# Optimization experiments

Hardware: AMD Instinct MI355X
Metric: run time of the kernel (lower is better)

## Reference

```python
import jax, jax.numpy as jnp
import numpy as np

B, T, C, H = 4, 4096, 512, 64  # batch, seq(patches), n_embed, head_size

def setup_inputs() -> dict:
    key = jax.random.key(0)
    kx, kk, kq, kv = jax.random.split(key, 4)
    x = jax.random.normal(kx, (B, T, C), dtype=jnp.float32)
    # torch nn.Linear(n_embed, head_size).weight is [H, C]; store transposed [C, H]
    Wk = jax.random.normal(kk, (C, H), dtype=jnp.float32) / np.sqrt(C)
    Wq = jax.random.normal(kq, (C, H), dtype=jnp.float32) / np.sqrt(C)
    Wv = jax.random.normal(kv, (C, H), dtype=jnp.float32) / np.sqrt(C)
    return {"x": x, "Wk": Wk, "Wq": Wq, "Wv": Wv}

def reference(x, Wk, Wq, Wv):
    Bn, Tn, Cn = x.shape
    k = x @ Wk  # [B,T,H]
    q = x @ Wq
    v = x @ Wv
    # NOTE: original scales by C**-0.5 with C = n_embed (input dim), not head_size
    scores = jnp.einsum('bth,bsh->bts', q, k) * (Cn ** -0.5)  # [B,T,T]
    causal = jnp.tril(jnp.ones((Tn, Tn), dtype=bool))
    scores = jnp.where(causal, scores, -jnp.inf)
    attn = jax.nn.softmax(scores, axis=-1)
    return jnp.einsum('bts,bsh->bth', attn, v)  # [B,T,H]
```

## Files before the change

kernel.cpp:

```cpp
#include <hip/hip_runtime.h>
#include <hip/hip_bf16.h>

#define Bb 4
#define Tt 4096

typedef __bf16 bf16;
typedef __attribute__((ext_vector_type(8))) __bf16 bf16x8;
typedef __attribute__((ext_vector_type(4))) __bf16 bf16x4;
typedef __attribute__((ext_vector_type(2))) __bf16 bf16x2;
typedef __attribute__((ext_vector_type(4))) float f32x4;
typedef __attribute__((ext_vector_type(2))) unsigned int u32x2;
typedef __attribute__((ext_vector_type(4))) unsigned int u32x4;


__global__ __launch_bounds__(256) void wt_kernel(const float* __restrict__ Wk,
                                                 const float* __restrict__ Wq,
                                                 const float* __restrict__ Wv,
                                                 bf16* __restrict__ wt) {
  int idx = blockIdx.x * 256 + threadIdx.x;
  int mat = idx >> 15;
  int rem = idx & 32767;
  int n = rem >> 9;
  int k = rem & 511;
  const float* W = (mat == 0) ? Wk : (mat == 1) ? Wq : Wv;
  float v = W[k * 64 + n];
  if (mat == 1) v *= 0.0637587165f;
  wt[idx] = (bf16)v;
}

__global__ __launch_bounds__(256) void proj_kernel(const float* __restrict__ x,
                                                   const bf16* __restrict__ wt,
                                                   bf16* __restrict__ Kb,
                                                   bf16* __restrict__ Qb,
                                                   bf16* __restrict__ VTb) {
  __shared__ __attribute__((aligned(16))) bf16 xs[16][520];
  int tid = threadIdx.x;
  int row0 = blockIdx.x * 16;

  int sr = tid >> 4, sc = (tid & 15) * 4;
  const float* xr = x + (size_t)(row0 + sr) * 512;
#pragma unroll
  for (int j = 0; j < 8; ++j) {
    f32x4 a = *(const f32x4*)(xr + sc + j * 64);
    bf16x4 h;
#pragma unroll
    for (int e = 0; e < 4; ++e) h[e] = (bf16)a[e];
    *(bf16x4*)&xs[sr][sc + j * 64] = h;
  }
  __syncthreads();

  int wave = tid >> 6, lane = tid & 63, m = lane & 15, quad = lane >> 4;
  f32x4 acc[3];
#pragma unroll
  for (int i = 0; i < 3; ++i) acc[i] = (f32x4){0.f, 0.f, 0.f, 0.f};

#pragma unroll 4
  for (int kk = 0; kk < 512; kk += 32) {
    bf16x8 af = *(const bf16x8*)&xs[m][kk + quad * 8];
#pragma unroll
    for (int i = 0; i < 3; ++i) {
      int nt = wave * 3 + i;
      bf16x8 bfr = *(const bf16x8*)(wt + (nt >> 2) * 32768 +
                                    (((nt & 3) * 16) + m) * 512 + kk + quad * 8);
      acc[i] = __builtin_amdgcn_mfma_f32_16x16x32_bf16(af, bfr, acc[i], 0, 0, 0);
    }
  }

  int b = row0 >> 12, tloc = row0 & 4095;
#pragma unroll
  for (int i = 0; i < 3; ++i) {
    int nt = wave * 3 + i, mat = nt >> 2, n0 = (nt & 3) * 16;
    if (mat == 2) {
      bf16x4 pv;
#pragma unroll
      for (int r = 0; r < 4; ++r) pv[r] = (bf16)acc[i][r];
      *(bf16x4*)&VTb[((size_t)b * 64 + n0 + m) * 4096 + tloc + quad * 4] = pv;
    } else {
      bf16* dst = (mat == 0) ? Kb : Qb;
#pragma unroll
      for (int r = 0; r < 4; ++r)
        dst[(size_t)(row0 + quad * 4 + r) * 64 + n0 + m] = (bf16)acc[i][r];
    }
  }
}

static __device__ inline unsigned pk2(float lo, float hi) {
  bf16x2 t;
  t[0] = (bf16)lo;
  t[1] = (bf16)hi;
  return __builtin_bit_cast(unsigned int, t);
}
static __device__ inline void plswap(unsigned& a, unsigned& b) {
  u32x2 r = __builtin_amdgcn_permlane16_swap(a, b, false, false);
  a = r.x;
  b = r.y;
}

__global__ __launch_bounds__(256, 4) void attn_kernel(const bf16* __restrict__ Qb,
                                                      const bf16* __restrict__ Kb,
                                                      const bf16* __restrict__ VTb,
                                                      bf16* __restrict__ Opart,
                                                      float* __restrict__ Lpart,
                                                      float* __restrict__ out) {
  __shared__ __attribute__((aligned(16))) bf16 Kt[2][64][72];
  __shared__ __attribute__((aligned(16))) bf16 Vt[2][64][72];

  int tid = threadIdx.x, wave = tid >> 6, lane = tid & 63;
  int m = lane & 15, quad = lane >> 4, kq = quad * 8;

  int uu = 1151 - (int)blockIdx.x;
  int b = uu / 288, u2 = uu % 288;
  int g = 0;
  while (u2 >= 4 * (g + 1) * (g + 2)) ++g;
  int rr = u2 - 4 * g * (g + 1);
  int qi = 8 * g + rr / (g + 1);
  int c = rr % (g + 1);
  int t0 = qi * 64;
  int s_beg = c * 512;
  int s_end = min(s_beg + 512, t0 + 64);
  int niter = (s_end - s_beg) >> 6;

  const bf16* Qp = Qb + ((size_t)b * Tt + t0 + wave * 16 + m) * 64;
  bf16x8 aq0 = *(const bf16x8*)(Qp + kq);
  bf16x8 aq1 = *(const bf16x8*)(Qp + 32 + kq);

  bf16x8 onesb;
#pragma unroll
  for (int j = 0; j < 8; ++j) onesb[j] = (bf16)1.0f;

  f32x4 o[4];
#pragma unroll
  for (int i = 0; i < 4; ++i) o[i] = (f32x4){0.f, 0.f, 0.f, 0.f};
  f32x4 lsum = (f32x4){0.f, 0.f, 0.f, 0.f};

  int r_ = tid >> 2, seg = tid & 3;
  const bf16* Kbase = Kb + (size_t)b * Tt * 64;
  const bf16* VTbase = VTb + (size_t)b * 64 * 4096;

  {
    const bf16* ks = Kbase + (size_t)(s_beg + r_) * 64 + seg * 16;
    bf16x8 k0 = *(const bf16x8*)ks;
    bf16x8 k1 = *(const bf16x8*)(ks + 8);
    const bf16* vs = VTbase + (size_t)r_ * 4096 + s_beg + seg * 16;
    bf16x8 v0 = *(const bf16x8*)vs;
    bf16x8 v1 = *(const bf16x8*)(vs + 8);
    *(bf16x8*)&Kt[0][r_][seg * 16] = k0;
    *(bf16x8*)&Kt[0][r_][seg * 16 + 8] = k1;
    *(bf16x8*)&Vt[0][r_][seg * 16] = v0;
    *(bf16x8*)&Vt[0][r_][seg * 16 + 8] = v1;
  }
  __syncthreads();

  int qrow = t0 + wave * 16 + m;

  for (int i = 0; i < niter; ++i) {
    int s0 = s_beg + i * 64;
    int cb = i & 1;
    bool more = (i + 1 < niter);

    bf16x8 k0, k1, v0, v1;
    if (more) {
      int sn = s0 + 64;
      const bf16* ks2 = Kbase + (size_t)(sn + r_) * 64 + seg * 16;
      k0 = *(const bf16x8*)ks2;
      k1 = *(const bf16x8*)(ks2 + 8);
      const bf16* vs2 = VTbase + (size_t)r_ * 4096 + sn + seg * 16;
      v0 = *(const bf16x8*)vs2;
      v1 = *(const bf16x8*)(vs2 + 8);
    }

    f32x4 s[4];
#pragma unroll
    for (int nt = 0; nt < 4; ++nt) {
      bf16x8 ak0 = *(const bf16x8*)&Kt[cb][nt * 16 + m][kq];
      bf16x8 ak1 = *(const bf16x8*)&Kt[cb][nt * 16 + m][32 + kq];
      f32x4 sa = (f32x4){0.f, 0.f, 0.f, 0.f};
      sa = __builtin_amdgcn_mfma_f32_16x16x32_bf16(ak0, aq0, sa, 0, 0, 0);
      sa = __builtin_amdgcn_mfma_f32_16x16x32_bf16(ak1, aq1, sa, 0, 0, 0);
      s[nt] = sa;
    }

    if (s0 + 64 > t0) {
      int kvb = s0 + 4 * quad;
#pragma unroll
      for (int nt = 0; nt < 4; ++nt)
#pragma unroll
        for (int r = 0; r < 4; ++r)
          if (kvb + nt * 16 + r > qrow) s[nt][r] = -1e30f;
    }

    unsigned pA[4], pB[4];
#pragma unroll
    for (int nt = 0; nt < 4; ++nt) {
      float e0 = __builtin_amdgcn_exp2f(s[nt][0]);
      float e1 = __builtin_amdgcn_exp2f(s[nt][1]);
      float e2 = __builtin_amdgcn_exp2f(s[nt][2]);
      float e3 = __builtin_amdgcn_exp2f(s[nt][3]);
      pA[nt] = pk2(e0, e1);
      pB[nt] = pk2(e2, e3);
    }

#pragma unroll
    for (int ch = 0; ch < 2; ++ch) {
      unsigned a0 = pA[2 * ch], a1 = pA[2 * ch + 1];
      unsigned c0 = pB[2 * ch], c1 = pB[2 * ch + 1];
      plswap(a0, a1);
      plswap(c0, c1);
      u32x4 uap = {a0, c0, a1, c1};
      bf16x8 ap = __builtin_bit_cast(bf16x8, uap);
      lsum = __builtin_amdgcn_mfma_f32_16x16x32_bf16(ap, onesb, lsum, 0, 0, 0);
      int fb8 = (4 * ch + 2 * (quad & 1) + (quad >> 1)) * 8;
#pragma unroll
      for (int nt = 0; nt < 4; ++nt) {
        bf16x8 bv = *(const bf16x8*)&Vt[cb][nt * 16 + m][fb8];
        o[nt] = __builtin_amdgcn_mfma_f32_16x16x32_bf16(ap, bv, o[nt], 0, 0, 0);
      }
    }

    if (more) {
      int nb = cb ^ 1;
      *(bf16x8*)&Kt[nb][r_][seg * 16] = k0;
      *(bf16x8*)&Kt[nb][r_][seg * 16 + 8] = k1;
      *(bf16x8*)&Vt[nb][r_][seg * 16] = v0;
      *(bf16x8*)&Vt[nb][r_][seg * 16 + 8] = v1;
      __syncthreads();
    }
  }

  int rl0 = wave * 16 + quad * 4;
  if (qi < 8) {
    float* op = out + ((size_t)b * Tt + t0) * 64;
#pragma unroll
    for (int r = 0; r < 4; ++r) {
      float inv = 1.0f / lsum[r];
#pragma unroll
      for (int nt = 0; nt < 4; ++nt)
        op[(size_t)(rl0 + r) * 64 + nt * 16 + m] = o[nt][r] * inv;
    }
  } else {
    int p = b * 288 + 4 * g * (g + 1) + (qi - 8 * g) * (g + 1) + c;
    bf16* Op = Opart + (size_t)p * 4096;
#pragma unroll
    for (int r = 0; r < 4; ++r)
#pragma unroll
      for (int nt = 0; nt < 4; ++nt)
        Op[(rl0 + r) * 64 + nt * 16 + m] = (bf16)o[nt][r];
    if (m == 0) {
#pragma unroll
      for (int r = 0; r < 4; ++r) Lpart[p * 64 + rl0 + r] = lsum[r];
    }
  }
}

__global__ __launch_bounds__(256) void combine_kernel(const bf16* __restrict__ Opart,
                                                      const float* __restrict__ Lpart,
                                                      float* __restrict__ out) {
  int blk = blockIdx.x;
  int b = blk / 224, rem = blk % 224;
  int qi = 8 + (rem >> 2), rq = rem & 3;
  int g = qi >> 3, nc = g + 1;
  int pb = b * 288 + 4 * g * (g + 1) + (qi - 8 * g) * (g + 1);
  int t = threadIdx.x, col = t & 63, rl = t >> 6;
#pragma unroll
  for (int rr = 0; rr < 4; ++rr) {
    int row64 = rq * 16 + rl * 4 + rr;
    float L = 0.f, acc = 0.f;
    for (int cc = 0; cc < nc; ++cc) {
      L += Lpart[(pb + cc) * 64 + row64];
      acc += (float)Opart[(size_t)(pb + cc) * 4096 + row64 * 64 + col];
    }
    out[((size_t)b * Tt + qi * 64 + row64) * 64 + col] = acc / L;
  }
}

extern "C" void kernel_launch(void* const* d_in, const int* in_sizes, int n_in,
                              void* d_out, int out_size, void* d_ws, size_t ws_size,
                              hipStream_t stream) {
  const float* x = (const float*)d_in[0];
  const float* Wk = (const float*)d_in[1];
  const float* Wq = (const float*)d_in[2];
  const float* Wv = (const float*)d_in[3];
  float* out = (float*)d_out;

  char* w = (char*)d_ws;
  bf16* wt = (bf16*)w;
  bf16* Kb = (bf16*)(w + 196608);
  bf16* Qb = (bf16*)(w + 2293760);
  bf16* VTb = (bf16*)(w + 4390912);
  bf16* Opart = (bf16*)(w + 6488064);
  float* Lpart = (float*)(w + 15925248);

  wt_kernel<<<384, 256, 0, stream>>>(Wk, Wq, Wv, wt);
  proj_kernel<<<1024, 256, 0, stream>>>(x, wt, Kb, Qb, VTb);
  attn_kernel<<<1152, 256, 0, stream>>>(Qb, Kb, VTb, Opart, Lpart, out);
  combine_kernel<<<896, 256, 0, stream>>>(Opart, Lpart, out);
}
```

Before: 134.4 us.

## Process two 64-row query tiles per attention block to reuse K/V tiles

Measured after the change: 131.7 us. 2.0% less time.

```diff
diff --git a/kernel.cpp b/kernel.cpp
--- a/kernel.cpp
+++ b/kernel.cpp
@@ -96,7 +96,7 @@
   b = r.y;
 }
 
-__global__ __launch_bounds__(256, 4) void attn_kernel(const bf16* __restrict__ Qb,
+__global__ __launch_bounds__(256, 3) void attn_kernel(const bf16* __restrict__ Qb,
                                                       const bf16* __restrict__ Kb,
                                                       const bf16* __restrict__ VTb,
                                                       bf16* __restrict__ Opart,
@@ -108,30 +108,36 @@
   int tid = threadIdx.x, wave = tid >> 6, lane = tid & 63;
   int m = lane & 15, quad = lane >> 4, kq = quad * 8;
 
-  int uu = 1151 - (int)blockIdx.x;
-  int b = uu / 288, u2 = uu % 288;
+  int uu = 575 - (int)blockIdx.x;
+  int b = uu / 144, u2 = uu % 144;
   int g = 0;
-  while (u2 >= 4 * (g + 1) * (g + 2)) ++g;
-  int rr = u2 - 4 * g * (g + 1);
-  int qi = 8 * g + rr / (g + 1);
+  while (u2 >= 2 * (g + 1) * (g + 2)) ++g;
+  int rr = u2 - 2 * g * (g + 1);
+  int qi2 = 4 * g + rr / (g + 1);
   int c = rr % (g + 1);
-  int t0 = qi * 64;
+  int t0 = qi2 * 128;
   int s_beg = c * 512;
-  int s_end = min(s_beg + 512, t0 + 64);
+  int s_end = min(s_beg + 512, t0 + 128);
   int niter = (s_end - s_beg) >> 6;
 
   const bf16* Qp = Qb + ((size_t)b * Tt + t0 + wave * 16 + m) * 64;
-  bf16x8 aq0 = *(const bf16x8*)(Qp + kq);
-  bf16x8 aq1 = *(const bf16x8*)(Qp + 32 + kq);
+  bf16x8 aq00 = *(const bf16x8*)(Qp + kq);
+  bf16x8 aq01 = *(const bf16x8*)(Qp + 32 + kq);
+  bf16x8 aq10 = *(const bf16x8*)(Qp + 4096 + kq);
+  bf16x8 aq11 = *(const bf16x8*)(Qp + 4096 + 32 + kq);
 
   bf16x8 onesb;
 #pragma unroll
   for (int j = 0; j < 8; ++j) onesb[j] = (bf16)1.0f;
 
-  f32x4 o[4];
-#pragma unroll
-  for (int i = 0; i < 4; ++i) o[i] = (f32x4){0.f, 0.f, 0.f, 0.f};
-  f32x4 lsum = (f32x4){0.f, 0.f, 0.f, 0.f};
+  f32x4 o0[4], o1[4];
+#pragma unroll
+  for (int i = 0; i < 4; ++i) {
+    o0[i] = (f32x4){0.f, 0.f, 0.f, 0.f};
+    o1[i] = (f32x4){0.f, 0.f, 0.f, 0.f};
+  }
+  f32x4 lsum0 = (f32x4){0.f, 0.f, 0.f, 0.f};
+  f32x4 lsum1 = (f32x4){0.f, 0.f, 0.f, 0.f};
 
   int r_ = tid >> 2, seg = tid & 3;
   const bf16* Kbase = Kb + (size_t)b * Tt * 64;
@@ -151,16 +157,16 @@
   }
   __syncthreads();
 
-  int qrow = t0 + wave * 16 + m;
+  int qrow0 = t0 + wave * 16 + m;
 
   for (int i = 0; i < niter; ++i) {
-    int s0 = s_beg + i * 64;
+    int kv0 = s_beg + i * 64;
     int cb = i & 1;
     bool more = (i + 1 < niter);
 
     bf16x8 k0, k1, v0, v1;
     if (more) {
-      int sn = s0 + 64;
+      int sn = kv0 + 64;
       const bf16* ks2 = Kbase + (size_t)(sn + r_) * 64 + seg * 16;
       k0 = *(const bf16x8*)ks2;
       k1 = *(const bf16x8*)(ks2 + 8);
@@ -169,52 +175,76 @@
       v1 = *(const bf16x8*)(vs2 + 8);
     }
 
-    f32x4 s[4];
+    f32x4 s0[4], s1[4];
 #pragma unroll
     for (int nt = 0; nt < 4; ++nt) {
       bf16x8 ak0 = *(const bf16x8*)&Kt[cb][nt * 16 + m][kq];
       bf16x8 ak1 = *(const bf16x8*)&Kt[cb][nt * 16 + m][32 + kq];
       f32x4 sa = (f32x4){0.f, 0.f, 0.f, 0.f};
-      sa = __builtin_amdgcn_mfma_f32_16x16x32_bf16(ak0, aq0, sa, 0, 0, 0);
-      sa = __builtin_amdgcn_mfma_f32_16x16x32_bf16(ak1, aq1, sa, 0, 0, 0);
-      s[nt] = sa;
-    }
-
-    if (s0 + 64 > t0) {
-      int kvb = s0 + 4 * quad;
+      sa = __builtin_amdgcn_mfma_f32_16x16x32_bf16(ak0, aq00, sa, 0, 0, 0);
+      sa = __builtin_amdgcn_mfma_f32_16x16x32_bf16(ak1, aq01, sa, 0, 0, 0);
+      s0[nt] = sa;
+      f32x4 sb = (f32x4){0.f, 0.f, 0.f, 0.f};
+      sb = __builtin_amdgcn_mfma_f32_16x16x32_bf16(ak0, aq10, sb, 0, 0, 0);
+      sb = __builtin_amdgcn_mfma_f32_16x16x32_bf16(ak1, aq11, sb, 0, 0, 0);
+      s1[nt] = sb;
+    }
+
+    if (kv0 + 64 > t0) {
+      int kvb = kv0 + 4 * quad;
 #pragma unroll
       for (int nt = 0; nt < 4; ++nt)
 #pragma unroll
         for (int r = 0; r < 4; ++r)
-          if (kvb + nt * 16 + r > qrow) s[nt][r] = -1e30f;
-    }
-
-    unsigned pA[4], pB[4];
+          if (kvb + nt * 16 + r > qrow0) s0[nt][r] = -1e30f;
+    }
+    if (kv0 >= t0 + 64) {
+      int kvb = kv0 + 4 * quad;
+#pragma unroll
+      for (int nt = 0; nt < 4; ++nt)
+#pragma unroll
+        for (int r = 0; r < 4; ++r)
+          if (kvb + nt * 16 + r > qrow0 + 64) s1[nt][r] = -1e30f;
+    }
+
+    unsigned pA0[4], pB0[4], pA1[4], pB1[4];
 #pragma unroll
     for (int nt = 0; nt < 4; ++nt) {
-      float e0 = __builtin_amdgcn_exp2f(s[nt][0]);
-      float e1 = __builtin_amdgcn_exp2f(s[nt][1]);
-      float e2 = __builtin_amdgcn_exp2f(s[nt][2]);
-      float e3 = __builtin_amdgcn_exp2f(s[nt][3]);
-      pA[nt] = pk2(e0, e1);
-      pB[nt] = pk2(e2, e3);
+      pA0[nt] = pk2(__builtin_amdgcn_exp2f(s0[nt][0]), __builtin_amdgcn_exp2f(s0[nt][1]));
+      pB0[nt] = pk2(__builtin_amdgcn_exp2f(s0[nt][2]), __builtin_amdgcn_exp2f(s0[nt][3]));
+      pA1[nt] = pk2(__builtin_amdgcn_exp2f(s1[nt][0]), __builtin_amdgcn_exp2f(s1[nt][1]));
+      pB1[nt] = pk2(__builtin_amdgcn_exp2f(s1[nt][2]), __builtin_amdgcn_exp2f(s1[nt][3]));
     }
 
 #pragma unroll
     for (int ch = 0; ch < 2; ++ch) {
-      unsigned a0 = pA[2 * ch], a1 = pA[2 * ch + 1];
-      unsigned c0 = pB[2 * ch], c1 = pB[2 * ch + 1];
+      unsigned a0 = pA0[2 * ch], a1 = pA0[2 * ch + 1];
+      unsigned c0 = pB0[2 * ch], c1 = pB0[2 * ch + 1];
       plswap(a0, a1);
       plswap(c0, c1);
-      u32x4 uap = {a0, c0, a1, c1};
-      bf16x8 ap = __builtin_bit_cast(bf16x8, uap);
-      lsum = __builtin_amdgcn_mfma_f32_16x16x32_bf16(ap, onesb, lsum, 0, 0, 0);
+      u32x4 ua0 = {a0, c0, a1, c1};
+      bf16x8 ap0 = __builtin_bit_cast(bf16x8, ua0);
+      lsum0 = __builtin_amdgcn_mfma_f32_16x16x32_bf16(ap0, onesb, lsum0, 0, 0, 0);
+
       int fb8 = (4 * ch + 2 * (quad & 1) + (quad >> 1)) * 8;
-#pragma unroll
-      for (int nt = 0; nt < 4; ++nt) {
-        bf16x8 bv = *(const bf16x8*)&Vt[cb][nt * 16 + m][fb8];
-        o[nt] = __builtin_amdgcn_mfma_f32_16x16x32_bf16(ap, bv, o[nt], 0, 0, 0);
-      }
+      bf16x8 bv[4];
+#pragma unroll
+      for (int nt = 0; nt < 4; ++nt)
+        bv[nt] = *(const bf16x8*)&Vt[cb][nt * 16 + m][fb8];
+#pragma unroll
+      for (int nt = 0; nt < 4; ++nt)
+        o0[nt] = __builtin_amdgcn_mfma_f32_16x16x32_bf16(ap0, bv[nt], o0[nt], 0, 0, 0);
+
+      unsigned b0 = pA1[2 * ch], b1 = pA1[2 * ch + 1];
+      unsigned d0 = pB1[2 * ch], d1 = pB1[2 * ch + 1];
+      plswap(b0, b1);
+      plswap(d0, d1);
+      u32x4 ua1 = {b0, d0, b1, d1};
+      bf16x8 ap1 = __builtin_bit_cast(bf16x8, ua1);
+      lsum1 = __builtin_amdgcn_mfma_f32_16x16x32_bf16(ap1, onesb, lsum1, 0, 0, 0);
+#pragma unroll
+      for (int nt = 0; nt < 4; ++nt)
+        o1[nt] = __builtin_amdgcn_mfma_f32_16x16x32_bf16(ap1, bv[nt], o1[nt], 0, 0, 0);
     }
 
     if (more) {
@@ -228,26 +258,34 @@
   }
 
   int rl0 = wave * 16 + quad * 4;
-  if (qi < 8) {
+  if (g == 0) {
     float* op = out + ((size_t)b * Tt + t0) * 64;
 #pragma unroll
     for (int r = 0; r < 4; ++r) {
-      float inv = 1.0f / lsum[r];
-#pragma unroll
-      for (int nt = 0; nt < 4; ++nt)
-        op[(size_t)(rl0 + r) * 64 + nt * 16 + m] = o[nt][r] * inv;
+      float inv0 = 1.0f / lsum0[r];
+      float inv1 = 1.0f / lsum1[r];
+#pragma unroll
+      for (int nt = 0; nt < 4; ++nt) {
+        op[(size_t)(rl0 + r) * 64 + nt * 16 + m] = o0[nt][r] * inv0;
+        op[(size_t)(64 + rl0 + r) * 64 + nt * 16 + m] = o1[nt][r] * inv1;
+      }
     }
   } else {
-    int p = b * 288 + 4 * g * (g + 1) + (qi - 8 * g) * (g + 1) + c;
-    bf16* Op = Opart + (size_t)p * 4096;
+    int p = b * 140 + u2 - 4;
+    bf16* Op = Opart + (size_t)p * 8192;
 #pragma unroll
     for (int r = 0; r < 4; ++r)
 #pragma unroll
-      for (int nt = 0; nt < 4; ++nt)
-        Op[(rl0 + r) * 64 + nt * 16 + m] = (bf16)o[nt][r];
+      for (int nt = 0; nt < 4; ++nt) {
+        Op[(rl0 + r) * 64 + nt * 16 + m] = (bf16)o0[nt][r];
+        Op[(64 + rl0 + r) * 64 + nt * 16 + m] = (bf16)o1[nt][r];
+      }
     if (m == 0) {
 #pragma unroll
-      for (int r = 0; r < 4; ++r) Lpart[p * 64 + rl0 + r] = lsum[r];
+      for (int r = 0; r < 4; ++r) {
+        Lpart[p * 128 + rl0 + r] = lsum0[r];
+        Lpart[p * 128 + 64 + rl0 + r] = lsum1[r];
+      }
     }
   }
 }
@@ -257,19 +295,20 @@
                                                       float* __restrict__ out) {
   int blk = blockIdx.x;
   int b = blk / 224, rem = blk % 224;
-  int qi = 8 + (rem >> 2), rq = rem & 3;
-  int g = qi >> 3, nc = g + 1;
-  int pb = b * 288 + 4 * g * (g + 1) + (qi - 8 * g) * (g + 1);
+  int qi2 = 4 + (rem >> 3), rq = rem & 7;
+  int g = qi2 >> 2, nc = g + 1;
+  int u2b = 2 * g * (g + 1) + (qi2 - 4 * g) * (g + 1);
+  int pb = b * 140 + u2b - 4;
   int t = threadIdx.x, col = t & 63, rl = t >> 6;
 #pragma unroll
   for (int rr = 0; rr < 4; ++rr) {
-    int row64 = rq * 16 + rl * 4 + rr;
+    int row128 = rq * 16 + rl * 4 + rr;
     float L = 0.f, acc = 0.f;
     for (int cc = 0; cc < nc; ++cc) {
-      L += Lpart[(pb + cc) * 64 + row64];
-      acc += (float)Opart[(size_t)(pb + cc) * 4096 + row64 * 64 + col];
-    }
-    out[((size_t)b * Tt + qi * 64 + row64) * 64 + col] = acc / L;
+      L += Lpart[(pb + cc) * 128 + row128];
+      acc += (float)Opart[(size_t)(pb + cc) * 8192 + row128 * 64 + col];
+    }
+    out[((size_t)b * Tt + qi2 * 128 + row128) * 64 + col] = acc / L;
   }
 }
 
@@ -292,6 +331,6 @@
 
   wt_kernel<<<384, 256, 0, stream>>>(Wk, Wq, Wv, wt);
   proj_kernel<<<1024, 256, 0, stream>>>(x, wt, Kb, Qb, VTb);
-  attn_kernel<<<1152, 256, 0, stream>>>(Qb, Kb, VTb, Opart, Lpart, out);
+  attn_kernel<<<576, 256, 0, stream>>>(Qb, Kb, VTb, Opart, Lpart, out);
   combine_kernel<<<896, 256, 0, stream>>>(Opart, Lpart, out);
 }
```
